# Kernel tuning notes

Hardware: AMD Instinct MI355X
Metric: run time of the kernel (lower is better)

Reference implementation:

```python
import jax, jax.numpy as jnp
import numpy as np

N_NODES = 50000
N_EDGES = 800000
N_GRAPHS = 64
IN_DIM, HID, OUT = 128, 128, 16


def gcn_conv(x, src, dst, deg_inv_sqrt, W, b):
    # x: [N, Cin]; src/dst: [E+N] (self-loops appended); W: [Cin, Cout]
    h = x @ W                                   # [N, Cout]
    norm = deg_inv_sqrt[src] * deg_inv_sqrt[dst]  # [E+N]
    msg = h[src] * norm[:, None]                # gather + scale
    out = jax.ops.segment_sum(msg, dst, num_segments=N_NODES)
    return out + b


def setup_inputs() -> dict:
    key = jax.random.key(0)
    ks = jax.random.split(key, 8)
    x = jax.random.normal(ks[0], (N_NODES, IN_DIM), dtype=jnp.float32)
    edge_index = jax.random.randint(ks[1], (2, N_EDGES), 0, N_NODES, dtype=jnp.int64)
    batch = jnp.sort(jax.random.randint(ks[2], (N_NODES,), 0, N_GRAPHS, dtype=jnp.int64))
    s = 1.0 / np.sqrt(IN_DIM)
    W1 = jax.random.normal(ks[3], (IN_DIM, HID), dtype=jnp.float32) * s
    b1 = jnp.zeros((HID,), dtype=jnp.float32)
    W2 = jax.random.normal(ks[4], (HID, HID), dtype=jnp.float32) * (1.0 / np.sqrt(HID))
    b2 = jnp.zeros((HID,), dtype=jnp.float32)
    Wfc = jax.random.normal(ks[5], (HID, OUT), dtype=jnp.float32) * (1.0 / np.sqrt(HID))
    bfc = jnp.zeros((OUT,), dtype=jnp.float32)
    return {"x": x, "edge_index": edge_index, "batch": batch,
            "W1": W1, "b1": b1, "W2": W2, "b2": b2, "Wfc": Wfc, "bfc": bfc}


def reference(x, edge_index, batch, W1, b1, W2, b2, Wfc, bfc):
    self_loops = jnp.arange(N_NODES, dtype=edge_index.dtype)
    src = jnp.concatenate([edge_index[0], self_loops])  # [E+N]
    dst = jnp.concatenate([edge_index[1], self_loops])
    deg = jax.ops.segment_sum(jnp.ones_like(dst, dtype=x.dtype), dst, num_segments=N_NODES)
    deg_inv_sqrt = jnp.where(deg > 0, jax.lax.rsqrt(deg), 0.0)

    h = jax.nn.relu(gcn_conv(x, src, dst, deg_inv_sqrt, W1, b1))
    h = jax.nn.relu(gcn_conv(h, src, dst, deg_inv_sqrt, W2, b2))

    # global mean pool over graphs
    sums = jax.ops.segment_sum(h, batch, num_segments=N_GRAPHS)         # [G, HID]
    cnts = jax.ops.segment_sum(jnp.ones((N_NODES,), h.dtype), batch, num_segments=N_GRAPHS)
    pooled = sums / jnp.maximum(cnts, 1.0)[:, None]

    return pooled @ Wfc + bfc  # [G, OUT]
```

## Files before the change

kernel.cpp:

```cpp
#include <hip/hip_runtime.h>
#include <math.h>

#define N_NODES 50000
#define N_EDGES 800000
#define N_GRAPHS 64
#define DIM 128
#define OUTD 16

#define BSHIFT 8
#define BNODES 256
#define NBUCK ((N_NODES + BNODES - 1) / BNODES)
#define TILE 2048
#define RCAP 8192
#define BSLOT 4864
#define GEMMB 256
#define BIN_GRID ((N_EDGES + TILE - 1) / TILE)

typedef __attribute__((ext_vector_type(8))) short short8;
typedef __attribute__((ext_vector_type(4))) float f32x4;

static __device__ __forceinline__ unsigned short f2bf(float f) {
    unsigned u = __float_as_uint(f);
    u += 0x7fffu + ((u >> 16) & 1u);
    return (unsigned short)(u >> 16);
}
static __device__ __forceinline__ float bfl(unsigned u) {
    return __uint_as_float(u << 16);
}
static __device__ __forceinline__ float bfh(unsigned u) {
    return __uint_as_float(u & 0xffff0000u);
}

__global__ __launch_bounds__(256) void k_init(int* __restrict__ bcnt,
                                              float* __restrict__ pool) {
    int tid = threadIdx.x;
    if (tid < NBUCK) bcnt[tid] = 0;
    for (int i = tid; i < N_GRAPHS * DIM; i += 256) pool[i] = 0.f;
}

template <int BF16IN>
static __device__ __forceinline__ void gemm_body(const void* __restrict__ Av,
                                                 const float* __restrict__ Wg,
                                                 unsigned short* __restrict__ C,
                                                 int nrows,
                                                 unsigned* smemW, unsigned* smemC,
                                                 int tile0, int tstride) {
    unsigned* Wl = smemW;
    {
        int t = threadIdx.x;
        int p = t & 63;
        int kp = p * 2;
        int n0 = (t >> 6) * 32;
        int kstep = kp >> 5;
        int quad = (kp >> 3) & 3;
        int jw = (kp & 7) >> 1;
        const float* r0 = Wg + (size_t)kp * DIM;
        const float* r1 = r0 + DIM;
        int rot = (p >> 2) & 7;
#pragma unroll
        for (int i4 = 0; i4 < 8; ++i4) {
            int nb = ((i4 + rot) & 7) * 4;
            int n = n0 + nb;
            float4 lo = *(const float4*)(r0 + n);
            float4 hi = *(const float4*)(r1 + n);
            const float* lp = &lo.x;
            const float* hp = &hi.x;
#pragma unroll
            for (int ii = 0; ii < 4; ++ii) {
                int nn = n + ii;
                int ct = nn >> 4;
                int l  = quad * 16 + (nn & 15);
                unsigned vlo = f2bf(lp[ii]);
                unsigned vhi = f2bf(hp[ii]);
                Wl[(((kstep * 8 + ct) * 64) + l) * 4 + jw] = vlo | (vhi << 16);
            }
        }
    }
    __syncthreads();

    int wid  = threadIdx.x >> 6;
    int lane = threadIdx.x & 63;
    int m    = lane & 15;
    int quad = lane >> 4;
    const short8* Wf = (const short8*)Wl;
    unsigned short* cs = (unsigned short*)smemC + wid * 4352;
    const unsigned char* cb = (const unsigned char*)smemC + wid * 8704;

    int ntiles = (nrows + 127) / 128;
    for (int tile = tile0; tile < ntiles; tile += tstride) {
        int row0 = tile * 128 + wid * 32;
        if (row0 >= nrows) continue;

        int rA = row0 + m;      if (rA >= nrows) rA = nrows - 1;
        int rB = row0 + 16 + m; if (rB >= nrows) rB = nrows - 1;

        short8 af0[4], af1[4];
        if (BF16IN) {
            const unsigned short* arowA = (const unsigned short*)Av + (size_t)rA * DIM + quad * 8;
            const unsigned short* arowB = (const unsigned short*)Av + (size_t)rB * DIM + quad * 8;
#pragma unroll
            for (int ks = 0; ks < 4; ++ks) {
                af0[ks] = *(const short8*)(arowA + ks * 32);
                af1[ks] = *(const short8*)(arowB + ks * 32);
            }
        } else {
            const float* arowA = (const float*)Av + (size_t)rA * DIM + quad * 8;
            const float* arowB = (const float*)Av + (size_t)rB * DIM + quad * 8;
#pragma unroll
            for (int ks = 0; ks < 4; ++ks) {
                float4 lo = *(const float4*)(arowA + ks * 32);
                float4 hi = *(const float4*)(arowA + ks * 32 + 4);
                short8 f;
                f[0] = (short)f2bf(lo.x); f[1] = (short)f2bf(lo.y);
                f[2] = (short)f2bf(lo.z); f[3] = (short)f2bf(lo.w);
                f[4] = (short)f2bf(hi.x); f[5] = (short)f2bf(hi.y);
                f[6] = (short)f2bf(hi.z); f[7] = (short)f2bf(hi.w);
                af0[ks] = f;
                lo = *(const float4*)(arowB + ks * 32);
                hi = *(const float4*)(arowB + ks * 32 + 4);
                f[0] = (short)f2bf(lo.x); f[1] = (short)f2bf(lo.y);
                f[2] = (short)f2bf(lo.z); f[3] = (short)f2bf(lo.w);
                f[4] = (short)f2bf(hi.x); f[5] = (short)f2bf(hi.y);
                f[6] = (short)f2bf(hi.z); f[7] = (short)f2bf(hi.w);
                af1[ks] = f;
            }
        }

        f32x4 acc0[8], acc1[8];
#pragma unroll
        for (int ct = 0; ct < 8; ++ct) {
            acc0[ct] = (f32x4){0.f, 0.f, 0.f, 0.f};
            acc1[ct] = (f32x4){0.f, 0.f, 0.f, 0.f};
        }

#pragma unroll
        for (int ks = 0; ks < 4; ++ks) {
#pragma unroll
            for (int ct = 0; ct < 8; ++ct) {
                short8 bfrag = Wf[(ks * 8 + ct) * 64 + lane];
                acc0[ct] = __builtin_amdgcn_mfma_f32_16x16x32_bf16(af0[ks], bfrag, acc0[ct], 0, 0, 0);
                acc1[ct] = __builtin_amdgcn_mfma_f32_16x16x32_bf16(af1[ks], bfrag, acc1[ct], 0, 0, 0);
            }
        }

#pragma unroll
        for (int ct = 0; ct < 8; ++ct) {
#pragma unroll
            for (int reg = 0; reg < 4; ++reg) {
                cs[(quad * 4 + reg) * 136 + ct * 16 + m]      = f2bf(acc0[ct][reg]);
                cs[(16 + quad * 4 + reg) * 136 + ct * 16 + m] = f2bf(acc1[ct][reg]);
            }
        }
#pragma unroll
        for (int i = 0; i < 8; ++i) {
            int rg = i * 4 + quad;
            int r = row0 + rg;
            if (r < nrows) {
                uint4 vv = *(const uint4*)(cb + rg * 272 + m * 16);
                *((uint4*)(C + (size_t)r * DIM) + m) = vv;
            }
        }
    }
}

__global__ __launch_bounds__(256) void k_fused1(const float* __restrict__ A,
                                                const float* __restrict__ Wg,
                                                unsigned short* __restrict__ C,
                                                int nrows,
                                                const int* __restrict__ src,
                                                const int* __restrict__ dstp,
                                                int* __restrict__ bcnt,
                                                unsigned* __restrict__ bucket_arr) {
    __shared__ unsigned smemW[32768 / 4];
    __shared__ unsigned smemC[34816 / 4];
    if (blockIdx.x >= GEMMB) {
        int* cnt  = (int*)smemW;
        int* base = cnt + NBUCK;
        int tile0 = (blockIdx.x - GEMMB) * TILE;
        for (int i = threadIdx.x; i < NBUCK; i += 256) cnt[i] = 0;
        __syncthreads();
#pragma unroll
        for (int j = 0; j < TILE / 512; ++j) {
            int e = tile0 + j * 512 + threadIdx.x * 2;
            if (e < N_EDGES) {
                int2 d = *(const int2*)(dstp + e);
                atomicAdd(&cnt[d.x >> BSHIFT], 1);
                atomicAdd(&cnt[d.y >> BSHIFT], 1);
            }
        }
        __syncthreads();
        for (int i = threadIdx.x; i < NBUCK; i += 256) {
            int c = cnt[i];
            base[i] = i * BSLOT + (c ? atomicAdd(&bcnt[i], c) : 0);
            cnt[i] = 0;
        }
        __syncthreads();
#pragma unroll
        for (int j = 0; j < TILE / 512; ++j) {
            int e = tile0 + j * 512 + threadIdx.x * 2;
            if (e < N_EDGES) {
                int2 s = *(const int2*)(src + e);
                int2 d = *(const int2*)(dstp + e);
                int b0 = d.x >> BSHIFT, b1 = d.y >> BSHIFT;
                int p0 = base[b0] + atomicAdd(&cnt[b0], 1);
                bucket_arr[p0] = (unsigned)s.x | ((unsigned)(d.x & 255) << 16);
                int p1 = base[b1] + atomicAdd(&cnt[b1], 1);
                bucket_arr[p1] = (unsigned)s.y | ((unsigned)(d.y & 255) << 16);
            }
        }
        return;
    }
    gemm_body<0>(A, Wg, C, nrows, smemW, smemC, blockIdx.x, GEMMB);
}

__global__ __launch_bounds__(256) void k_gemm2(const unsigned short* __restrict__ A,
                                               const float* __restrict__ Wg,
                                               unsigned short* __restrict__ C,
                                               int nrows) {
    __shared__ unsigned smemW[32768 / 4];
    __shared__ unsigned smemC[34816 / 4];
    gemm_body<1>(A, Wg, C, nrows, smemW, smemC, blockIdx.x, gridDim.x);
}

__global__ __launch_bounds__(256) void k_binB(const unsigned* __restrict__ barr,
                                              const int* __restrict__ bcnt,
                                              int* __restrict__ row_off,
                                              float* __restrict__ dis,
                                              unsigned short* __restrict__ csr) {
    __shared__ unsigned raw[RCAP];
    __shared__ unsigned short stage[RCAP];
    __shared__ int hist[BNODES];
    __shared__ int scn[BNODES];
    __shared__ int borig[256], bscan[256];
    int tid = threadIdx.x;
    int b = blockIdx.x;
    int n0 = b << BSHIFT;

    int cv = (tid < NBUCK) ? bcnt[tid] : 0;
    borig[tid] = cv;
    bscan[tid] = cv;
    __syncthreads();
    for (int off = 1; off < 256; off <<= 1) {
        int t = (tid >= off) ? bscan[tid - off] : 0;
        __syncthreads();
        bscan[tid] += t;
        __syncthreads();
    }
    int rbase = bscan[b] - borig[b];
    int len = borig[b];
    const unsigned* bin = barr + (size_t)b * BSLOT;

    hist[tid] = 0;
    __syncthreads();
    for (int i = tid; i < len; i += 256) {
        unsigned ed = bin[i];
        if (i < RCAP) raw[i] = ed;
        atomicAdd(&hist[ed >> 16], 1);
    }
    __syncthreads();
    int v = hist[tid];
    scn[tid] = v;
    __syncthreads();
    for (int off = 1; off < 256; off <<= 1) {
        int t = (tid >= off) ? scn[tid - off] : 0;
        __syncthreads();
        scn[tid] += t;
        __syncthreads();
    }
    int excl = scn[tid] - v;
    int n = n0 + tid;
    if (n < N_NODES) {
        row_off[n] = rbase + excl;
        dis[n] = rsqrtf((float)(v + 1));
    }
    if (b == NBUCK - 1 && tid == 0) row_off[N_NODES] = N_EDGES;
    hist[tid] = excl;
    __syncthreads();
    for (int i = tid; i < len; i += 256) {
        unsigned ed = (i < RCAP) ? raw[i] : bin[i];
        int p = atomicAdd(&hist[ed >> 16], 1);
        unsigned short sv = (unsigned short)(ed & 0xffffu);
        if (p < RCAP) stage[p] = sv;
        else csr[rbase + p] = sv;
    }
    __syncthreads();
    int lim = min(len, RCAP);
    for (int i = tid; i < lim; i += 256)
        csr[rbase + i] = stage[i];
}

template <int FUSE_POOL>
__global__ __launch_bounds__(256) void k_agg(const uint4* __restrict__ Hb4,
                                             const int* __restrict__ row_off,
                                             const unsigned short* __restrict__ csr,
                                             const float* __restrict__ dis,
                                             const float* __restrict__ bias,
                                             uint4* __restrict__ out,
                                             const int* __restrict__ batch,
                                             float* __restrict__ pool) {
    __shared__ float sacc[16][DIM];
    __shared__ int sg[16];
    int lane = threadIdx.x & 15;
    int nl   = threadIdx.x >> 4;
    int node = blockIdx.x * 16 + nl;
    if (node >= N_NODES) return;

    float dn = dis[node];
    float wself = dn * dn;
    uint4 hp = Hb4[(size_t)node * 16 + lane];
    float a0[8], a1[8], a2[8], a3[8];
    a0[0] = wself * bfl(hp.x); a0[1] = wself * bfh(hp.x);
    a0[2] = wself * bfl(hp.y); a0[3] = wself * bfh(hp.y);
    a0[4] = wself * bfl(hp.z); a0[5] = wself * bfh(hp.z);
    a0[6] = wself * bfl(hp.w); a0[7] = wself * bfh(hp.w);
#pragma unroll
    for (int j = 0; j < 8; ++j) { a1[j] = 0.f; a2[j] = 0.f; a3[j] = 0.f; }

    int e = row_off[node], e1 = row_off[node + 1];
    for (; e + 4 <= e1; e += 4) {
        int s0 = csr[e];     int s1 = csr[e + 1];
        int s2 = csr[e + 2]; int s3 = csr[e + 3];
        uint4 g0 = Hb4[(size_t)s0 * 16 + lane];
        uint4 g1 = Hb4[(size_t)s1 * 16 + lane];
        uint4 g2 = Hb4[(size_t)s2 * 16 + lane];
        uint4 g3 = Hb4[(size_t)s3 * 16 + lane];
        float w0 = dn * dis[s0], w1 = dn * dis[s1];
        float w2 = dn * dis[s2], w3 = dn * dis[s3];
        a0[0] = fmaf(w0, bfl(g0.x), a0[0]); a0[1] = fmaf(w0, bfh(g0.x), a0[1]);
        a0[2] = fmaf(w0, bfl(g0.y), a0[2]); a0[3] = fmaf(w0, bfh(g0.y), a0[3]);
        a0[4] = fmaf(w0, bfl(g0.z), a0[4]); a0[5] = fmaf(w0, bfh(g0.z), a0[5]);
        a0[6] = fmaf(w0, bfl(g0.w), a0[6]); a0[7] = fmaf(w0, bfh(g0.w), a0[7]);
        a1[0] = fmaf(w1, bfl(g1.x), a1[0]); a1[1] = fmaf(w1, bfh(g1.x), a1[1]);
        a1[2] = fmaf(w1, bfl(g1.y), a1[2]); a1[3] = fmaf(w1, bfh(g1.y), a1[3]);
        a1[4] = fmaf(w1, bfl(g1.z), a1[4]); a1[5] = fmaf(w1, bfh(g1.z), a1[5]);
        a1[6] = fmaf(w1, bfl(g1.w), a1[6]); a1[7] = fmaf(w1, bfh(g1.w), a1[7]);
        a2[0] = fmaf(w2, bfl(g2.x), a2[0]); a2[1] = fmaf(w2, bfh(g2.x), a2[1]);
        a2[2] = fmaf(w2, bfl(g2.y), a2[2]); a2[3] = fmaf(w2, bfh(g2.y), a2[3]);
        a2[4] = fmaf(w2, bfl(g2.z), a2[4]); a2[5] = fmaf(w2, bfh(g2.z), a2[5]);
        a2[6] = fmaf(w2, bfl(g2.w), a2[6]); a2[7] = fmaf(w2, bfh(g2.w), a2[7]);
        a3[0] = fmaf(w3, bfl(g3.x), a3[0]); a3[1] = fmaf(w3, bfh(g3.x), a3[1]);
        a3[2] = fmaf(w3, bfl(g3.y), a3[2]); a3[3] = fmaf(w3, bfh(g3.y), a3[3]);
        a3[4] = fmaf(w3, bfl(g3.z), a3[4]); a3[5] = fmaf(w3, bfh(g3.z), a3[5]);
        a3[6] = fmaf(w3, bfl(g3.w), a3[6]); a3[7] = fmaf(w3, bfh(g3.w), a3[7]);
    }
    for (; e < e1; ++e) {
        int s = csr[e];
        uint4 g = Hb4[(size_t)s * 16 + lane];
        float w = dn * dis[s];
        a0[0] = fmaf(w, bfl(g.x), a0[0]); a0[1] = fmaf(w, bfh(g.x), a0[1]);
        a0[2] = fmaf(w, bfl(g.y), a0[2]); a0[3] = fmaf(w, bfh(g.y), a0[3]);
        a0[4] = fmaf(w, bfl(g.z), a0[4]); a0[5] = fmaf(w, bfh(g.z), a0[5]);
        a0[6] = fmaf(w, bfl(g.w), a0[6]); a0[7] = fmaf(w, bfh(g.w), a0[7]);
    }

    float4 b0 = ((const float4*)bias)[lane * 2];
    float4 b1v = ((const float4*)bias)[lane * 2 + 1];
    float r[8];
    r[0] = fmaxf(a0[0] + a1[0] + a2[0] + a3[0] + b0.x, 0.f);
    r[1] = fmaxf(a0[1] + a1[1] + a2[1] + a3[1] + b0.y, 0.f);
    r[2] = fmaxf(a0[2] + a1[2] + a2[2] + a3[2] + b0.z, 0.f);
    r[3] = fmaxf(a0[3] + a1[3] + a2[3] + a3[3] + b0.w, 0.f);
    r[4] = fmaxf(a0[4] + a1[4] + a2[4] + a3[4] + b1v.x, 0.f);
    r[5] = fmaxf(a0[5] + a1[5] + a2[5] + a3[5] + b1v.y, 0.f);
    r[6] = fmaxf(a0[6] + a1[6] + a2[6] + a3[6] + b1v.z, 0.f);
    r[7] = fmaxf(a0[7] + a1[7] + a2[7] + a3[7] + b1v.w, 0.f);

    if (!FUSE_POOL) {
        uint4 ov;
        ov.x = (unsigned)f2bf(r[0]) | ((unsigned)f2bf(r[1]) << 16);
        ov.y = (unsigned)f2bf(r[2]) | ((unsigned)f2bf(r[3]) << 16);
        ov.z = (unsigned)f2bf(r[4]) | ((unsigned)f2bf(r[5]) << 16);
        ov.w = (unsigned)f2bf(r[6]) | ((unsigned)f2bf(r[7]) << 16);
        out[(size_t)node * 16 + lane] = ov;
    } else {
#pragma unroll
        for (int j = 0; j < 8; ++j) sacc[nl][lane * 8 + j] = r[j];
        if (lane == 0) sg[nl] = batch[node];
        __syncthreads();
        int c = threadIdx.x;
        if (c < DIM) {
            float acc = 0.f;
            int curg = sg[0];
#pragma unroll
            for (int n = 0; n < 16; ++n) {
                int g = sg[n];
                if (g != curg) {
                    atomicAdd(&pool[curg * DIM + c], acc);
                    acc = 0.f; curg = g;
                }
                acc += sacc[n][c];
            }
            atomicAdd(&pool[curg * DIM + c], acc);
        }
    }
}

__global__ void k_fc(const float* __restrict__ pool, const int* __restrict__ batch,
                     const float* __restrict__ Wfc, const float* __restrict__ bfc,
                     float* __restrict__ out) {
    int id = blockIdx.x * blockDim.x + threadIdx.x;
    if (id >= N_GRAPHS * OUTD) return;
    int g = id >> 4, o = id & 15;
    int lo = 0, hi = N_NODES;
    while (lo < hi) { int mid = (lo + hi) >> 1; if (batch[mid] < g) lo = mid + 1; else hi = mid; }
    int l0 = lo;
    lo = 0; hi = N_NODES;
    while (lo < hi) { int mid = (lo + hi) >> 1; if (batch[mid] < g + 1) lo = mid + 1; else hi = mid; }
    int cntg = lo - l0;
    float inv = 1.0f / fmaxf((float)cntg, 1.0f);
    float acc = bfc[o];
    const float* p = pool + g * DIM;
    for (int c = 0; c < DIM; ++c)
        acc = fmaf(p[c] * inv, Wfc[c * OUTD + o], acc);
    out[id] = acc;
}


extern "C" void kernel_launch(void* const* d_in, const int* in_sizes, int n_in,
                              void* d_out, int out_size, void* d_ws, size_t ws_size,
                              hipStream_t stream) {
    const float* x    = (const float*)d_in[0];
    const int*   ei   = (const int*)d_in[1];
    const int*   batch= (const int*)d_in[2];
    const float* W1   = (const float*)d_in[3];
    const float* b1   = (const float*)d_in[4];
    const float* W2   = (const float*)d_in[5];
    const float* b2   = (const float*)d_in[6];
    const float* Wfc  = (const float*)d_in[7];
    const float* bfc  = (const float*)d_in[8];
    float* out = (float*)d_out;

    char* ws = (char*)d_ws;
    size_t off = 0;
    auto alloc = [&](size_t bytes) -> char* {
        char* p = ws + off;
        off = (off + bytes + 255) & ~(size_t)255;
        return p;
    };
    int*      bcnt     = (int*)     alloc((size_t)NBUCK * 4);
    int*      row_off  = (int*)     alloc((size_t)(N_NODES + 1) * 4);
    float*    dis      = (float*)   alloc((size_t)N_NODES * 4);
    unsigned short* csr= (unsigned short*)alloc((size_t)N_EDGES * 2);
    unsigned* barr     = (unsigned*)alloc((size_t)NBUCK * BSLOT * 4);
    float*    pool     = (float*)   alloc((size_t)N_GRAPHS * DIM * 4);
    unsigned short* Hb = (unsigned short*)alloc((size_t)N_NODES * DIM * 2);
    unsigned short* Hb2= (unsigned short*)alloc((size_t)N_NODES * DIM * 2);

    const int* src = ei;
    const int* dst = ei + N_EDGES;

    k_init<<<1, 256, 0, stream>>>(bcnt, pool);
    k_fused1<<<GEMMB + BIN_GRID, 256, 0, stream>>>(x, W1, Hb, N_NODES,
                                                   src, dst, bcnt, barr);
    k_binB<<<NBUCK, 256, 0, stream>>>(barr, bcnt, row_off, dis, csr);

    int agg_grid = (N_NODES + 15) / 16;
    k_agg<0><<<agg_grid, 256, 0, stream>>>((const uint4*)Hb, row_off, csr, dis, b1,
                                           (uint4*)Hb2, batch, pool);
    k_gemm2<<<GEMMB, 256, 0, stream>>>(Hb2, W2, Hb, N_NODES);
    k_agg<1><<<agg_grid, 256, 0, stream>>>((const uint4*)Hb, row_off, csr, dis, b2,
                                           nullptr, batch, pool);
    k_fc<<<(N_GRAPHS * OUTD + 255) / 256, 256, 0, stream>>>(pool, batch, Wfc, bfc, out);
}
```

Measured before the change: 203.9 us.

## Fuse second-layer GEMM into first aggregation epilogue via MFMA

```diff
diff --git a/kernel.cpp b/kernel.cpp
--- a/kernel.cpp
+++ b/kernel.cpp
@@ -32,10 +32,24 @@
 }
 
 __global__ __launch_bounds__(256) void k_init(int* __restrict__ bcnt,
-                                              float* __restrict__ pool) {
+                                              float* __restrict__ pool,
+                                              const float* __restrict__ W2,
+                                              unsigned* __restrict__ W2f) {
     int tid = threadIdx.x;
     if (tid < NBUCK) bcnt[tid] = 0;
     for (int i = tid; i < N_GRAPHS * DIM; i += 256) pool[i] = 0.f;
+    for (int idx = tid; idx < (DIM / 2) * DIM; idx += 256) {
+        int kp = idx >> 7;
+        int n  = idx & 127;
+        int k  = kp * 2;
+        int kstep = kp >> 4;
+        int quad  = (kp >> 2) & 3;
+        int jw    = kp & 3;
+        int ct    = n >> 4;
+        unsigned vlo = f2bf(W2[(size_t)k * DIM + n]);
+        unsigned vhi = f2bf(W2[(size_t)(k + 1) * DIM + n]);
+        W2f[(((kstep * 8 + ct) * 64) + quad * 16 + (n & 15)) * 4 + jw] = vlo | (vhi << 16);
+    }
 }
 
 template <int BF16IN>
@@ -213,15 +227,6 @@
     gemm_body<0>(A, Wg, C, nrows, smemW, smemC, blockIdx.x, GEMMB);
 }
 
-__global__ __launch_bounds__(256) void k_gemm2(const unsigned short* __restrict__ A,
-                                               const float* __restrict__ Wg,
-                                               unsigned short* __restrict__ C,
-                                               int nrows) {
-    __shared__ unsigned smemW[32768 / 4];
-    __shared__ unsigned smemC[34816 / 4];
-    gemm_body<1>(A, Wg, C, nrows, smemW, smemC, blockIdx.x, gridDim.x);
-}
-
 __global__ __launch_bounds__(256) void k_binB(const unsigned* __restrict__ barr,
                                               const int* __restrict__ bcnt,
                                               int* __restrict__ row_off,
@@ -289,7 +294,7 @@
         csr[rbase + i] = stage[i];
 }
 
-template <int FUSE_POOL>
+template <int MODE>
 __global__ __launch_bounds__(256) void k_agg(const uint4* __restrict__ Hb4,
                                              const int* __restrict__ row_off,
                                              const unsigned short* __restrict__ csr,
@@ -297,13 +302,12 @@
                                              const float* __restrict__ bias,
                                              uint4* __restrict__ out,
                                              const int* __restrict__ batch,
-                                             float* __restrict__ pool) {
-    __shared__ float sacc[16][DIM];
-    __shared__ int sg[16];
+                                             float* __restrict__ pool,
+                                             const short8* __restrict__ W2f) {
+    __shared__ unsigned char smem[8768];
     int lane = threadIdx.x & 15;
     int nl   = threadIdx.x >> 4;
     int node = blockIdx.x * 16 + nl;
-    if (node >= N_NODES) return;
 
     float dn = dis[node];
     float wself = dn * dn;
@@ -365,16 +369,55 @@
     r[6] = fmaxf(a0[6] + a1[6] + a2[6] + a3[6] + b1v.z, 0.f);
     r[7] = fmaxf(a0[7] + a1[7] + a2[7] + a3[7] + b1v.w, 0.f);
 
-    if (!FUSE_POOL) {
-        uint4 ov;
-        ov.x = (unsigned)f2bf(r[0]) | ((unsigned)f2bf(r[1]) << 16);
-        ov.y = (unsigned)f2bf(r[2]) | ((unsigned)f2bf(r[3]) << 16);
-        ov.z = (unsigned)f2bf(r[4]) | ((unsigned)f2bf(r[5]) << 16);
-        ov.w = (unsigned)f2bf(r[6]) | ((unsigned)f2bf(r[7]) << 16);
-        out[(size_t)node * 16 + lane] = ov;
+    if (MODE == 2) {
+        unsigned short* sA = (unsigned short*)smem;
+        unsigned short* sC = (unsigned short*)smem + 2176;
+        uint4 av;
+        av.x = (unsigned)f2bf(r[0]) | ((unsigned)f2bf(r[1]) << 16);
+        av.y = (unsigned)f2bf(r[2]) | ((unsigned)f2bf(r[3]) << 16);
+        av.z = (unsigned)f2bf(r[4]) | ((unsigned)f2bf(r[5]) << 16);
+        av.w = (unsigned)f2bf(r[6]) | ((unsigned)f2bf(r[7]) << 16);
+        *(uint4*)(sA + nl * 136 + lane * 8) = av;
+        __syncthreads();
+
+        int wid = threadIdx.x >> 6;
+        int l64 = threadIdx.x & 63;
+        int m   = l64 & 15;
+        int q   = l64 >> 4;
+        short8 af[4];
+#pragma unroll
+        for (int ks = 0; ks < 4; ++ks)
+            af[ks] = *(const short8*)(sA + m * 136 + ks * 32 + q * 8);
+        f32x4 acc[2];
+        acc[0] = (f32x4){0.f, 0.f, 0.f, 0.f};
+        acc[1] = (f32x4){0.f, 0.f, 0.f, 0.f};
+#pragma unroll
+        for (int ks = 0; ks < 4; ++ks) {
+#pragma unroll
+            for (int j = 0; j < 2; ++j) {
+                int ct = wid * 2 + j;
+                short8 bfrag = W2f[(ks * 8 + ct) * 64 + l64];
+                acc[j] = __builtin_amdgcn_mfma_f32_16x16x32_bf16(af[ks], bfrag, acc[j], 0, 0, 0);
+            }
+        }
+#pragma unroll
+        for (int j = 0; j < 2; ++j) {
+#pragma unroll
+            for (int reg = 0; reg < 4; ++reg)
+                sC[(q * 4 + reg) * 136 + (wid * 2 + j) * 16 + m] = f2bf(acc[j][reg]);
+        }
+        __syncthreads();
+        {
+            int t = threadIdx.x;
+            int row = t >> 4, ch = t & 15;
+            uint4 vv = *(const uint4*)((const unsigned char*)sC + row * 272 + ch * 16);
+            out[(size_t)(blockIdx.x * 16 + row) * 16 + ch] = vv;
+        }
     } else {
-#pragma unroll
-        for (int j = 0; j < 8; ++j) sacc[nl][lane * 8 + j] = r[j];
+        float* sacc = (float*)smem;
+        int* sg = (int*)(smem + 16 * DIM * 4);
+#pragma unroll
+        for (int j = 0; j < 8; ++j) sacc[nl * DIM + lane * 8 + j] = r[j];
         if (lane == 0) sg[nl] = batch[node];
         __syncthreads();
         int c = threadIdx.x;
@@ -388,7 +431,7 @@
                     atomicAdd(&pool[curg * DIM + c], acc);
                     acc = 0.f; curg = g;
                 }
-                acc += sacc[n][c];
+                acc += sacc[n * DIM + c];
             }
             atomicAdd(&pool[curg * DIM + c], acc);
         }
@@ -443,22 +486,22 @@
     unsigned short* csr= (unsigned short*)alloc((size_t)N_EDGES * 2);
     unsigned* barr     = (unsigned*)alloc((size_t)NBUCK * BSLOT * 4);
     float*    pool     = (float*)   alloc((size_t)N_GRAPHS * DIM * 4);
+    unsigned* W2f      = (unsigned*)alloc((size_t)(DIM / 2) * DIM * 4);
     unsigned short* Hb = (unsigned short*)alloc((size_t)N_NODES * DIM * 2);
     unsigned short* Hb2= (unsigned short*)alloc((size_t)N_NODES * DIM * 2);
 
     const int* src = ei;
     const int* dst = ei + N_EDGES;
 
-    k_init<<<1, 256, 0, stream>>>(bcnt, pool);
+    k_init<<<1, 256, 0, stream>>>(bcnt, pool, W2, W2f);
     k_fused1<<<GEMMB + BIN_GRID, 256, 0, stream>>>(x, W1, Hb, N_NODES,
                                                    src, dst, bcnt, barr);
     k_binB<<<NBUCK, 256, 0, stream>>>(barr, bcnt, row_off, dis, csr);
 
     int agg_grid = (N_NODES + 15) / 16;
-    k_agg<0><<<agg_grid, 256, 0, stream>>>((const uint4*)Hb, row_off, csr, dis, b1,
-                                           (uint4*)Hb2, batch, pool);
-    k_gemm2<<<GEMMB, 256, 0, stream>>>(Hb2, W2, Hb, N_NODES);
-    k_agg<1><<<agg_grid, 256, 0, stream>>>((const uint4*)Hb, row_off, csr, dis, b2,
-                                           nullptr, batch, pool);
+    k_agg<2><<<agg_grid, 256, 0, stream>>>((const uint4*)Hb, row_off, csr, dis, b1,
+                                           (uint4*)Hb2, batch, pool, (const short8*)W2f);
+    k_agg<1><<<agg_grid, 256, 0, stream>>>((const uint4*)Hb2, row_off, csr, dis, b2,
+                                           nullptr, batch, pool, nullptr);
     k_fc<<<(N_GRAPHS * OUTD + 255) / 256, 256, 0, stream>>>(pool, batch, Wfc, bfc, out);
 }
```

Result: faster. 197.3 us (-3.2%).
